# Performance work log

Measured on AMD Instinct MI355X. Metric: run time of the kernel, lower is better.

Reference implementation:

```python
import jax, jax.numpy as jnp
import numpy as np

N, E, G, H, V, L = 100000, 1000000, 1000, 128, 64, 4
NEG_SLOPE = 0.2

def lrelu(x):
    return jnp.where(x >= 0, x, NEG_SLOPE * x)

def setup_inputs() -> dict:
    key = jax.random.key(0)
    ks = jax.random.split(key, 24)
    s = 0.05
    inp = {
        'nfeats': jax.random.randint(ks[0], (N, 9), 0, V, dtype=jnp.int32),
        'efeats': jax.random.randint(ks[1], (E, 3), 0, 4, dtype=jnp.int32),
        'src': jax.random.randint(ks[2], (E,), 0, N, dtype=jnp.int32),
        'dst': jax.random.randint(ks[3], (E,), 0, N, dtype=jnp.int32),
        'graph_ids': jnp.sort(jax.random.randint(ks[4], (N,), 0, G, dtype=jnp.int32)),
        'atom_emb': jax.random.normal(ks[5], (9, V, H), jnp.float32) * s,
        'Wq': jax.random.normal(ks[6], (L, H, H), jnp.float32) * s,
        'bq': jnp.zeros((L, H), jnp.float32),
        'Wk': jax.random.normal(ks[7], (L, H, H), jnp.float32) * s,
        'bk': jnp.zeros((L, H), jnp.float32),
        'Wr': jax.random.normal(ks[8], (L, H, H), jnp.float32) * s,
        'br': jnp.zeros((L, H), jnp.float32),
        'W1': jax.random.normal(ks[9], (H, H // 2), jnp.float32) * s,
        'b1': jnp.zeros((H // 2,), jnp.float32),
        'g1': jnp.ones((H // 2,), jnp.float32),
        'beta1': jnp.zeros((H // 2,), jnp.float32),
        'W2': jax.random.normal(ks[10], (H // 2, H // 4), jnp.float32) * s,
        'b2': jnp.zeros((H // 4,), jnp.float32),
        'g2': jnp.ones((H // 4,), jnp.float32),
        'beta2': jnp.zeros((H // 4,), jnp.float32),
        'W3': jax.random.normal(ks[11], (H // 4, 1), jnp.float32) * s,
        'b3': jnp.zeros((1,), jnp.float32),
    }
    return inp

def batchnorm(x, g, b):
    mu = jnp.mean(x, axis=0)
    var = jnp.var(x, axis=0)
    return (x - mu) * jax.lax.rsqrt(var + 1e-5) * g + b

def reference(nfeats, efeats, src, dst, graph_ids, atom_emb, Wq, bq, Wk, bk, Wr, br,
              W1, b1, g1, beta1, W2, b2, g2, beta2, W3, b3):
    # AtomEncoder: sum of per-feature embeddings -> [N, H]
    h = jnp.sum(atom_emb[jnp.arange(9)[None, :], nfeats], axis=1)
    for l in range(L):
        q = h @ Wq[l] + bq[l]            # dst-side transform [N,H]
        k = h @ Wk[l] + bk[l]            # src-side transform [N,H]
        m = lrelu(q[dst] + k[src])       # per-edge message [E,H]
        agg = jax.ops.segment_sum(m, dst, num_segments=N)  # [N,H]
        h = lrelu(agg @ Wr[l] + br[l])   # norm='none' -> identity, then activation
    hg = jax.ops.segment_sum(h, graph_ids, num_segments=G)  # sum pooling [G,H]
    x = lrelu(batchnorm(hg @ W1 + b1, g1, beta1))
    x = lrelu(batchnorm(x @ W2 + b2, g2, beta2))
    return x @ W3 + b3
```

## Files before the change

kernel.cpp:

```cpp
#include <hip/hip_runtime.h>

#define NN 100000
#define NP 100096
#define NE 1000000
#define NG 1000
#define H 128
#define NLAYER 4
#define NEG 0.2f
#define SCAN_BLOCKS 98

using short8 = __attribute__((ext_vector_type(8))) short;
using fx4 = __attribute__((ext_vector_type(4))) float;

__device__ __forceinline__ float lrelu(float x) { return x >= 0.f ? x : NEG * x; }

__device__ __forceinline__ unsigned short f2bf(float f) {
    union { float f; unsigned int u; } v;
    v.f = f;
    return (unsigned short)((v.u + 0x7fffu + ((v.u >> 16) & 1u)) >> 16);
}
__device__ __forceinline__ float bflo(unsigned int u) {
    union { unsigned int x; float f; } v;
    v.x = u << 16;
    return v.f;
}
__device__ __forceinline__ float bfhi(unsigned int u) {
    union { unsigned int x; float f; } v;
    v.x = u & 0xffff0000u;
    return v.f;
}

__global__ __launch_bounds__(256) void k_wt(const float* __restrict__ Wq,
                                            const float* __restrict__ Wk,
                                            const float* __restrict__ Wr,
                                            unsigned short* __restrict__ WT) {
    int mat = blockIdx.x;
    int l = mat / 3;
    int kind = mat - l * 3;
    const float* src = (kind == 0 ? Wq : kind == 1 ? Wk : Wr) + (size_t)l * H * H;
    unsigned short* dst = WT + (size_t)mat * H * H;
    for (int idx = threadIdx.x; idx < H * H; idx += 256) {
        int kk = idx >> 7, n = idx & 127;
        dst[n * H + kk] = f2bf(src[idx]);
    }
}

__global__ __launch_bounds__(256) void k_hist(const int* __restrict__ dst, int* __restrict__ deg) {
    int i = blockIdx.x * blockDim.x + threadIdx.x;
    if (i * 4 >= NE) return;
    int4 d = *(const int4*)(dst + i * 4);
    atomicAdd(&deg[d.x], 1);
    atomicAdd(&deg[d.y], 1);
    atomicAdd(&deg[d.z], 1);
    atomicAdd(&deg[d.w], 1);
}

__global__ __launch_bounds__(1024) void k_scan1(const int* __restrict__ deg,
                                                int* __restrict__ rowp,
                                                int* __restrict__ bsum) {
    __shared__ int tmp[1024];
    int t = threadIdx.x;
    int i = blockIdx.x * 1024 + t;
    int v = (i < NN) ? deg[i] : 0;
    tmp[t] = v;
    __syncthreads();
    for (int off = 1; off < 1024; off <<= 1) {
        int u = (t >= off) ? tmp[t - off] : 0;
        __syncthreads();
        tmp[t] += u;
        __syncthreads();
    }
    if (i < NN) rowp[i] = tmp[t] - v;
    if (t == 1023) bsum[blockIdx.x] = tmp[1023];
}

__global__ __launch_bounds__(128) void k_scan2(int* __restrict__ bsum) {
    __shared__ int tmp[128];
    int t = threadIdx.x;
    int v = (t < SCAN_BLOCKS) ? bsum[t] : 0;
    tmp[t] = v;
    __syncthreads();
    for (int off = 1; off < 128; off <<= 1) {
        int u = (t >= off) ? tmp[t - off] : 0;
        __syncthreads();
        tmp[t] += u;
        __syncthreads();
    }
    if (t < SCAN_BLOCKS) bsum[t] = tmp[t] - v;
}

#define SCAN3_BLOCKS ((NN + 255) / 256)
__global__ __launch_bounds__(256) void k_scan3g(const int* __restrict__ bsum,
                                                int* __restrict__ rowp,
                                                int* __restrict__ cursor,
                                                const int* __restrict__ gid,
                                                int* __restrict__ gstart) {
    int bid = blockIdx.x;
    int t = threadIdx.x;
    if (bid < SCAN3_BLOCKS) {
        int i = bid * 256 + t;
        if (i < NN) {
            int v = rowp[i] + bsum[i >> 10];
            rowp[i] = v;
            cursor[i] = v;
        }
        if (i == 0) rowp[NN] = NE;
    } else {
        int g = (bid - SCAN3_BLOCKS) * 256 + t;
        if (g > NG) return;
        if (g == NG) { gstart[NG] = NN; return; }
        int lo = 0, hi = NN;
        while (lo < hi) {
            int mid = (lo + hi) >> 1;
            if (gid[mid] < g) lo = mid + 1; else hi = mid;
        }
        gstart[g] = lo;
    }
}

__global__ __launch_bounds__(256) void k_scatter(const int* __restrict__ src,
                                                 const int* __restrict__ dst,
                                                 int* __restrict__ cursor,
                                                 int* __restrict__ csr_src) {
    int i = blockIdx.x * blockDim.x + threadIdx.x;
    if (i * 4 >= NE) return;
    int4 s = *(const int4*)(src + i * 4);
    int4 d = *(const int4*)(dst + i * 4);
    __builtin_nontemporal_store(s.x, &csr_src[atomicAdd(&cursor[d.x], 1)]);
    __builtin_nontemporal_store(s.y, &csr_src[atomicAdd(&cursor[d.y], 1)]);
    __builtin_nontemporal_store(s.z, &csr_src[atomicAdd(&cursor[d.z], 1)]);
    __builtin_nontemporal_store(s.w, &csr_src[atomicAdd(&cursor[d.w], 1)]);
}

__global__ __launch_bounds__(256) void k_aqk_mfma(const int* __restrict__ nfeats,
                                                  const float* __restrict__ emb,
                                                  const unsigned short* __restrict__ WTq,
                                                  const float* __restrict__ bq,
                                                  const unsigned short* __restrict__ WTk,
                                                  const float* __restrict__ bk,
                                                  unsigned short* __restrict__ q,
                                                  unsigned short* __restrict__ k) {
    __shared__ unsigned short hls[4][32][136];
    __shared__ int nf[128 * 9];
    int t = threadIdx.x;
    int lane = t & 63;
    int wave = t >> 6;
    int row0 = blockIdx.x * 128 + wave * 32;
    int lrow = lane & 15;
    int lk = (lane >> 4) << 3;
    unsigned short (*S)[136] = hls[wave];

    {
        int gbase = blockIdx.x * 128 * 9;
        for (int i = t; i < 128 * 9; i += 256) {
            int gi = gbase + i;
            nf[i] = nfeats[gi < NN * 9 ? gi : NN * 9 - 1];
        }
    }
    __syncthreads();

    {
        int c = lane * 2;
        const int* nfw = nf + wave * 32 * 9;
        for (int rr = 0; rr < 32; rr += 2) {
            float ax0 = 0.f, ay0 = 0.f, ax1 = 0.f, ay1 = 0.f;
#pragma unroll
            for (int f = 0; f < 9; ++f) {
                int i0 = nfw[rr * 9 + f];
                int i1 = nfw[(rr + 1) * 9 + f];
                float2 e0 = *(const float2*)(emb + (size_t)((f << 6) + i0) * H + c);
                float2 e1 = *(const float2*)(emb + (size_t)((f << 6) + i1) * H + c);
                ax0 += e0.x; ay0 += e0.y;
                ax1 += e1.x; ay1 += e1.y;
            }
            *(unsigned int*)&S[rr][c] = (unsigned int)f2bf(ax0) | ((unsigned int)f2bf(ay0) << 16);
            *(unsigned int*)&S[rr + 1][c] = (unsigned int)f2bf(ax1) | ((unsigned int)f2bf(ay1) << 16);
        }
    }

    short8 a[2][4];
#pragma unroll
    for (int rt = 0; rt < 2; ++rt)
#pragma unroll
        for (int ks = 0; ks < 4; ++ks)
            a[rt][ks] = *(const short8*)&S[rt * 16 + lrow][ks * 32 + lk];

#pragma unroll
    for (int pass = 0; pass < 4; ++pass) {
        const unsigned short* W = (pass < 2) ? WTq : WTk;
        const float* b = (pass < 2) ? bq : bk;
        unsigned short* o = (pass < 2) ? q : k;
        int c0 = (pass & 1) * 4;
        fx4 acc[2][4];
#pragma unroll
        for (int ct = 0; ct < 4; ++ct) {
            float v = b[(c0 + ct) * 16 + lrow];
#pragma unroll
            for (int rt = 0; rt < 2; ++rt) acc[rt][ct] = fx4{v, v, v, v};
        }
#pragma unroll
        for (int ks = 0; ks < 4; ++ks)
#pragma unroll
            for (int ct = 0; ct < 4; ++ct) {
                short8 w = *(const short8*)(W + ((c0 + ct) * 16 + lrow) * H + ks * 32 + lk);
#pragma unroll
                for (int rt = 0; rt < 2; ++rt)
                    acc[rt][ct] = __builtin_amdgcn_mfma_f32_16x16x32_bf16(a[rt][ks], w, acc[rt][ct], 0, 0, 0);
            }
#pragma unroll
        for (int rt = 0; rt < 2; ++rt)
#pragma unroll
            for (int ct = 0; ct < 4; ++ct)
#pragma unroll
                for (int rg = 0; rg < 4; ++rg)
                    S[rt * 16 + ((lane >> 4) << 2) + rg][(c0 + ct) * 16 + lrow] = f2bf(acc[rt][ct][rg]);
#pragma unroll
        for (int step = 0; step < 4; ++step) {
            int cch = step * 64 + lane;
            int r = cch >> 3;
            int off = c0 * 16 + (cch & 7) * 8;
            int gr = row0 + r;
            if (gr < NN)
                *(uint4*)(o + (size_t)gr * H + off) = *(const uint4*)&S[r][off];
        }
    }
}

__global__ __launch_bounds__(256) void k_r_mfma(const unsigned short* __restrict__ agg,
                                                const unsigned short* __restrict__ WTr,
                                                const float* __restrict__ br,
                                                unsigned short* __restrict__ hout) {
    __shared__ unsigned short hls[4][32][136];
    int lane = threadIdx.x & 63;
    int wave = threadIdx.x >> 6;
    int row0 = blockIdx.x * 128 + wave * 32;
    int lrow = lane & 15;
    int lk = (lane >> 4) << 3;
    unsigned short (*S)[136] = hls[wave];

    short8 a[2][4];
#pragma unroll
    for (int rt = 0; rt < 2; ++rt)
#pragma unroll
        for (int ks = 0; ks < 4; ++ks)
            a[rt][ks] = *(const short8*)(agg + (size_t)(row0 + rt * 16 + lrow) * H + ks * 32 + lk);

#pragma unroll
    for (int chf = 0; chf < 2; ++chf) {
        int c0 = chf * 4;
        fx4 acc[2][4];
#pragma unroll
        for (int ct = 0; ct < 4; ++ct) {
            float v = br[(c0 + ct) * 16 + lrow];
#pragma unroll
            for (int rt = 0; rt < 2; ++rt) acc[rt][ct] = fx4{v, v, v, v};
        }
#pragma unroll
        for (int ks = 0; ks < 4; ++ks)
#pragma unroll
            for (int ct = 0; ct < 4; ++ct) {
                short8 w = *(const short8*)(WTr + ((c0 + ct) * 16 + lrow) * H + ks * 32 + lk);
#pragma unroll
                for (int rt = 0; rt < 2; ++rt)
                    acc[rt][ct] = __builtin_amdgcn_mfma_f32_16x16x32_bf16(a[rt][ks], w, acc[rt][ct], 0, 0, 0);
            }
#pragma unroll
        for (int rt = 0; rt < 2; ++rt)
#pragma unroll
            for (int ct = 0; ct < 4; ++ct)
#pragma unroll
                for (int rg = 0; rg < 4; ++rg)
                    S[rt * 16 + ((lane >> 4) << 2) + rg][(c0 + ct) * 16 + lrow] = f2bf(lrelu(acc[rt][ct][rg]));
    }
#pragma unroll
    for (int step = 0; step < 8; ++step) {
        int cch = step * 64 + lane;
        int r = cch >> 4;
        int off = (cch & 15) * 8;
        int gr = row0 + r;
        if (gr < NN)
            *(uint4*)(hout + (size_t)gr * H + off) = *(const uint4*)&S[r][off];
    }
}

__global__ __launch_bounds__(256) void k_rqk_mfma(const unsigned short* __restrict__ agg,
                                                  const unsigned short* __restrict__ WTr,
                                                  const float* __restrict__ br,
                                                  const unsigned short* __restrict__ WTq,
                                                  const float* __restrict__ bq,
                                                  const unsigned short* __restrict__ WTk,
                                                  const float* __restrict__ bk,
                                                  unsigned short* __restrict__ q,
                                                  unsigned short* __restrict__ k) {
    __shared__ unsigned short hls[4][32][136];
    int lane = threadIdx.x & 63;
    int wave = threadIdx.x >> 6;
    int row0 = blockIdx.x * 128 + wave * 32;
    int lrow = lane & 15;
    int lk = (lane >> 4) << 3;
    unsigned short (*S)[136] = hls[wave];

    short8 a[2][4];
#pragma unroll
    for (int rt = 0; rt < 2; ++rt)
#pragma unroll
        for (int ks = 0; ks < 4; ++ks)
            a[rt][ks] = *(const short8*)(agg + (size_t)(row0 + rt * 16 + lrow) * H + ks * 32 + lk);

#pragma unroll
    for (int chf = 0; chf < 2; ++chf) {
        int c0 = chf * 4;
        fx4 acc[2][4];
#pragma unroll
        for (int ct = 0; ct < 4; ++ct) {
            float v = br[(c0 + ct) * 16 + lrow];
#pragma unroll
            for (int rt = 0; rt < 2; ++rt) acc[rt][ct] = fx4{v, v, v, v};
        }
#pragma unroll
        for (int ks = 0; ks < 4; ++ks)
#pragma unroll
            for (int ct = 0; ct < 4; ++ct) {
                short8 w = *(const short8*)(WTr + ((c0 + ct) * 16 + lrow) * H + ks * 32 + lk);
#pragma unroll
                for (int rt = 0; rt < 2; ++rt)
                    acc[rt][ct] = __builtin_amdgcn_mfma_f32_16x16x32_bf16(a[rt][ks], w, acc[rt][ct], 0, 0, 0);
            }
#pragma unroll
        for (int rt = 0; rt < 2; ++rt)
#pragma unroll
            for (int ct = 0; ct < 4; ++ct)
#pragma unroll
                for (int rg = 0; rg < 4; ++rg)
                    S[rt * 16 + ((lane >> 4) << 2) + rg][(c0 + ct) * 16 + lrow] = f2bf(lrelu(acc[rt][ct][rg]));
    }

    short8 a2[2][4];
#pragma unroll
    for (int rt = 0; rt < 2; ++rt)
#pragma unroll
        for (int ks = 0; ks < 4; ++ks)
            a2[rt][ks] = *(const short8*)&S[rt * 16 + lrow][ks * 32 + lk];

#pragma unroll
    for (int pass = 0; pass < 4; ++pass) {
        const unsigned short* W = (pass < 2) ? WTq : WTk;
        const float* b = (pass < 2) ? bq : bk;
        unsigned short* o = (pass < 2) ? q : k;
        int c0 = (pass & 1) * 4;
        fx4 acc[2][4];
#pragma unroll
        for (int ct = 0; ct < 4; ++ct) {
            float v = b[(c0 + ct) * 16 + lrow];
#pragma unroll
            for (int rt = 0; rt < 2; ++rt) acc[rt][ct] = fx4{v, v, v, v};
        }
#pragma unroll
        for (int ks = 0; ks < 4; ++ks)
#pragma unroll
            for (int ct = 0; ct < 4; ++ct) {
                short8 w = *(const short8*)(W + ((c0 + ct) * 16 + lrow) * H + ks * 32 + lk);
#pragma unroll
                for (int rt = 0; rt < 2; ++rt)
                    acc[rt][ct] = __builtin_amdgcn_mfma_f32_16x16x32_bf16(a2[rt][ks], w, acc[rt][ct], 0, 0, 0);
            }
#pragma unroll
        for (int rt = 0; rt < 2; ++rt)
#pragma unroll
            for (int ct = 0; ct < 4; ++ct)
#pragma unroll
                for (int rg = 0; rg < 4; ++rg)
                    S[rt * 16 + ((lane >> 4) << 2) + rg][(c0 + ct) * 16 + lrow] = f2bf(acc[rt][ct][rg]);
#pragma unroll
        for (int step = 0; step < 4; ++step) {
            int cch = step * 64 + lane;
            int r = cch >> 3;
            int off = c0 * 16 + (cch & 7) * 8;
            int gr = row0 + r;
            if (gr < NN)
                *(uint4*)(o + (size_t)gr * H + off) = *(const uint4*)&S[r][off];
        }
    }
}

__global__ __launch_bounds__(256) void k_agg(const unsigned short* __restrict__ q,
                                             const unsigned short* __restrict__ kk,
                                             const int* __restrict__ rowp,
                                             const int* __restrict__ csr_src,
                                             unsigned short* __restrict__ agg) {
    int node = blockIdx.x * 4 + (threadIdx.x >> 6);
    if (node >= NN) return;
    int lane = threadIdx.x & 63;
    int qt = lane >> 4;
    int ql = lane & 15;
    int start = rowp[node];
    int end = rowp[node + 1];

    uint4 qp = *(const uint4*)(q + (size_t)node * H + ql * 8);
    float qv0 = bflo(qp.x), qv1 = bfhi(qp.x), qv2 = bflo(qp.y), qv3 = bfhi(qp.y);
    float qv4 = bflo(qp.z), qv5 = bfhi(qp.z), qv6 = bflo(qp.w), qv7 = bfhi(qp.w);
    float a0 = 0.f, a1 = 0.f, a2 = 0.f, a3 = 0.f, a4 = 0.f, a5 = 0.f, a6 = 0.f, a7 = 0.f;

    for (int base = start; base < end; base += 64) {
        int cnt = end - base;
        if (cnt > 64) cnt = 64;
        int sid = (lane < cnt) ? csr_src[base + lane] : 0;
        int cnt16 = (cnt + 15) & ~15;
        for (int j = 0; j < cnt16; j += 16) {
            int jj0 = j + qt;
            int jj1 = j + 4 + qt;
            int jj2 = j + 8 + qt;
            int jj3 = j + 12 + qt;
            int s0 = __shfl(sid, jj0);
            int s1 = __shfl(sid, jj1);
            int s2 = __shfl(sid, jj2);
            int s3 = __shfl(sid, jj3);
            uint4 kp0 = *(const uint4*)(kk + (size_t)s0 * H + ql * 8);
            uint4 kp1 = *(const uint4*)(kk + (size_t)s1 * H + ql * 8);
            uint4 kp2 = *(const uint4*)(kk + (size_t)s2 * H + ql * 8);
            uint4 kp3 = *(const uint4*)(kk + (size_t)s3 * H + ql * 8);
            if (jj0 < cnt) {
                a0 += lrelu(qv0 + bflo(kp0.x)); a1 += lrelu(qv1 + bfhi(kp0.x));
                a2 += lrelu(qv2 + bflo(kp0.y)); a3 += lrelu(qv3 + bfhi(kp0.y));
                a4 += lrelu(qv4 + bflo(kp0.z)); a5 += lrelu(qv5 + bfhi(kp0.z));
                a6 += lrelu(qv6 + bflo(kp0.w)); a7 += lrelu(qv7 + bfhi(kp0.w));
            }
            if (jj1 < cnt) {
                a0 += lrelu(qv0 + bflo(kp1.x)); a1 += lrelu(qv1 + bfhi(kp1.x));
                a2 += lrelu(qv2 + bflo(kp1.y)); a3 += lrelu(qv3 + bfhi(kp1.y));
                a4 += lrelu(qv4 + bflo(kp1.z)); a5 += lrelu(qv5 + bfhi(kp1.z));
                a6 += lrelu(qv6 + bflo(kp1.w)); a7 += lrelu(qv7 + bfhi(kp1.w));
            }
            if (jj2 < cnt) {
                a0 += lrelu(qv0 + bflo(kp2.x)); a1 += lrelu(qv1 + bfhi(kp2.x));
                a2 += lrelu(qv2 + bflo(kp2.y)); a3 += lrelu(qv3 + bfhi(kp2.y));
                a4 += lrelu(qv4 + bflo(kp2.z)); a5 += lrelu(qv5 + bfhi(kp2.z));
                a6 += lrelu(qv6 + bflo(kp2.w)); a7 += lrelu(qv7 + bfhi(kp2.w));
            }
            if (jj3 < cnt) {
                a0 += lrelu(qv0 + bflo(kp3.x)); a1 += lrelu(qv1 + bfhi(kp3.x));
                a2 += lrelu(qv2 + bflo(kp3.y)); a3 += lrelu(qv3 + bfhi(kp3.y));
                a4 += lrelu(qv4 + bflo(kp3.z)); a5 += lrelu(qv5 + bfhi(kp3.z));
                a6 += lrelu(qv6 + bflo(kp3.w)); a7 += lrelu(qv7 + bfhi(kp3.w));
            }
        }
    }
    a0 += __shfl_xor(a0, 16); a0 += __shfl_xor(a0, 32);
    a1 += __shfl_xor(a1, 16); a1 += __shfl_xor(a1, 32);
    a2 += __shfl_xor(a2, 16); a2 += __shfl_xor(a2, 32);
    a3 += __shfl_xor(a3, 16); a3 += __shfl_xor(a3, 32);
    a4 += __shfl_xor(a4, 16); a4 += __shfl_xor(a4, 32);
    a5 += __shfl_xor(a5, 16); a5 += __shfl_xor(a5, 32);
    a6 += __shfl_xor(a6, 16); a6 += __shfl_xor(a6, 32);
    a7 += __shfl_xor(a7, 16); a7 += __shfl_xor(a7, 32);
    if (qt == 0) {
        uint4 o;
        o.x = (unsigned int)f2bf(a0) | ((unsigned int)f2bf(a1) << 16);
        o.y = (unsigned int)f2bf(a2) | ((unsigned int)f2bf(a3) << 16);
        o.z = (unsigned int)f2bf(a4) | ((unsigned int)f2bf(a5) << 16);
        o.w = (unsigned int)f2bf(a6) | ((unsigned int)f2bf(a7) << 16);
        *(uint4*)(agg + (size_t)node * H + ql * 8) = o;
    }
}

__global__ __launch_bounds__(256) void k_pool_seg(const unsigned short* __restrict__ h,
                                                  const int* __restrict__ gstart,
                                                  float* __restrict__ hg) {
    int g = blockIdx.x * 4 + (threadIdx.x >> 6);
    if (g >= NG) return;
    int lane = threadIdx.x & 63;
    int s = gstart[g], e = gstart[g + 1];
    float ax = 0.f, ay = 0.f;
    for (int n = s; n < e; ++n) {
        unsigned int hp = *(const unsigned int*)(h + (size_t)n * H + lane * 2);
        ax += bflo(hp);
        ay += bfhi(hp);
    }
    float2 o;
    o.x = ax;
    o.y = ay;
    *(float2*)(hg + (size_t)g * H + lane * 2) = o;
}

__global__ __launch_bounds__(256) void k_mlp1(const float* __restrict__ hg,
                                              const float* __restrict__ W1,
                                              const float* __restrict__ b1,
                                              float* __restrict__ x1) {
    __shared__ float W1s[128 * 64];
    __shared__ float hgs[4 * 128];
    int t = threadIdx.x;
    int g0 = blockIdx.x * 4;
#pragma unroll
    for (int i = 0; i < 32; ++i) W1s[t + i * 256] = W1[t + i * 256];
    for (int i = t; i < 4 * 128; i += 256) hgs[i] = hg[(size_t)g0 * H + i];
    __syncthreads();
    int g = t >> 6, c = t & 63;
    float acc = b1[c];
    const float* row = hgs + g * 128;
    for (int j = 0; j < 128; ++j) acc += row[j] * W1s[j * 64 + c];
    x1[(g0 + g) * 64 + c] = acc;
}

template <int C>
__global__ __launch_bounds__(1024) void k_bnstats(const float* __restrict__ x,
                                                  float* __restrict__ stats) {
    __shared__ float red[1024];
    __shared__ float mus[C];
    int t = threadIdx.x;
    int c = t & (C - 1), rc = t / C;
    const int R = 1024 / C;
    float s = 0.f;
    for (int g = rc; g < NG; g += R) s += x[g * C + c];
    red[t] = s;
    __syncthreads();
    if (t < C) {
        float S = 0.f;
        for (int i = 0; i < R; ++i) S += red[i * C + t];
        float mu = S / NG;
        mus[t] = mu;
        stats[t] = mu;
    }
    __syncthreads();
    float mu = mus[c];
    float s2 = 0.f;
    for (int g = rc; g < NG; g += R) {
        float d = x[g * C + c] - mu;
        s2 += d * d;
    }
    red[t] = s2;
    __syncthreads();
    if (t < C) {
        float Q = 0.f;
        for (int i = 0; i < R; ++i) Q += red[i * C + t];
        stats[C + t] = rsqrtf(Q / NG + 1e-5f);
    }
}

__global__ __launch_bounds__(256) void k_mlp2f(const float* __restrict__ x1,
                                               const float* __restrict__ st,
                                               const float* __restrict__ g1,
                                               const float* __restrict__ be1,
                                               const float* __restrict__ W2,
                                               const float* __restrict__ b2,
                                               float* __restrict__ x2) {
    __shared__ float W2s[64 * 32];
    __shared__ float x1s[8 * 64];
    int t = threadIdx.x;
    int g0 = blockIdx.x * 8;
#pragma unroll
    for (int i = 0; i < 8; ++i) W2s[t + i * 256] = W2[t + i * 256];
#pragma unroll
    for (int i = 0; i < 2; ++i) {
        int idx = t + i * 256;
        int c = idx & 63;
        float v = x1[(size_t)g0 * 64 + idx];
        v = (v - st[c]) * st[64 + c] * g1[c] + be1[c];
        x1s[idx] = lrelu(v);
    }
    __syncthreads();
    int g = t >> 5, c = t & 31;
    float acc = b2[c];
    const float* row = x1s + g * 64;
    for (int j = 0; j < 64; ++j) acc += row[j] * W2s[j * 32 + c];
    x2[(g0 + g) * 32 + c] = acc;
}

__global__ __launch_bounds__(256) void k_mlp3f(const float* __restrict__ x2,
                                               const float* __restrict__ st,
                                               const float* __restrict__ g2,
                                               const float* __restrict__ be2,
                                               const float* __restrict__ W3,
                                               const float* __restrict__ b3,
                                               float* __restrict__ out) {
    int g = blockIdx.x * blockDim.x + threadIdx.x;
    if (g >= NG) return;
    float acc = b3[0];
    for (int j = 0; j < 32; ++j) {
        float v = (x2[g * 32 + j] - st[j]) * st[32 + j] * g2[j] + be2[j];
        acc += lrelu(v) * W3[j];
    }
    out[g] = acc;
}

extern "C" void kernel_launch(void* const* d_in, const int* in_sizes, int n_in,
                              void* d_out, int out_size, void* d_ws, size_t ws_size,
                              hipStream_t stream) {
    const int* nfeats = (const int*)d_in[0];
    const int* src = (const int*)d_in[2];
    const int* dst = (const int*)d_in[3];
    const int* gid = (const int*)d_in[4];
    const float* emb = (const float*)d_in[5];
    const float* Wq = (const float*)d_in[6];
    const float* bq = (const float*)d_in[7];
    const float* Wk = (const float*)d_in[8];
    const float* bk = (const float*)d_in[9];
    const float* Wr = (const float*)d_in[10];
    const float* br = (const float*)d_in[11];
    const float* W1 = (const float*)d_in[12];
    const float* b1 = (const float*)d_in[13];
    const float* g1 = (const float*)d_in[14];
    const float* be1 = (const float*)d_in[15];
    const float* W2 = (const float*)d_in[16];
    const float* b2 = (const float*)d_in[17];
    const float* g2 = (const float*)d_in[18];
    const float* be2 = (const float*)d_in[19];
    const float* W3 = (const float*)d_in[20];
    const float* b3 = (const float*)d_in[21];
    float* out = (float*)d_out;

    size_t nh = (size_t)NP * H;
    unsigned short* P0 = (unsigned short*)d_ws;
    unsigned short* P1 = P0 + nh;
    unsigned short* P2 = P1 + nh;
    unsigned short* WT = P2 + nh;
    float* hg = (float*)(WT + 12 * H * H);
    float* x1 = hg + (size_t)NG * H;
    float* x2 = x1 + (size_t)NG * 64;
    float* st = x2 + (size_t)NG * 32;
    int* cursor = (int*)(st + 2 * 64);
    int* rowp = cursor + NN;
    int* bsum = rowp + NN + 1;
    int* csr_src = bsum + 128;
    int* gstart = csr_src + NE;

    hipMemsetAsync(cursor, 0, NN * sizeof(int), stream);
    k_hist<<<(NE / 4 + 255) / 256, 256, 0, stream>>>(dst, cursor);
    k_scan1<<<SCAN_BLOCKS, 1024, 0, stream>>>(cursor, rowp, bsum);
    k_scan2<<<1, 128, 0, stream>>>(bsum);
    k_scan3g<<<SCAN3_BLOCKS + 4, 256, 0, stream>>>(bsum, rowp, cursor, gid, gstart);
    k_scatter<<<(NE / 4 + 255) / 256, 256, 0, stream>>>(src, dst, cursor, csr_src);

    k_wt<<<12, 256, 0, stream>>>(Wq, Wk, Wr, WT);

    const int NB = NP / 128;
    k_aqk_mfma<<<NB, 256, 0, stream>>>(nfeats, emb, WT + 0 * H * H, bq, WT + 1 * H * H, bk, P1, P2);
    for (int l = 0; l < NLAYER; ++l) {
        k_agg<<<(NN + 3) / 4, 256, 0, stream>>>(P1, P2, rowp, csr_src, P0);
        if (l < NLAYER - 1) {
            k_rqk_mfma<<<NB, 256, 0, stream>>>(P0, WT + (size_t)(l * 3 + 2) * H * H, br + l * H,
                                               WT + (size_t)((l + 1) * 3 + 0) * H * H, bq + (l + 1) * H,
                                               WT + (size_t)((l + 1) * 3 + 1) * H * H, bk + (l + 1) * H,
                                               P1, P2);
        } else {
            k_r_mfma<<<NB, 256, 0, stream>>>(P0, WT + (size_t)(l * 3 + 2) * H * H, br + l * H, P1);
        }
    }

    k_pool_seg<<<(NG + 3) / 4, 256, 0, stream>>>(P1, gstart, hg);

    k_mlp1<<<NG / 4, 256, 0, stream>>>(hg, W1, b1, x1);
    k_bnstats<64><<<1, 1024, 0, stream>>>(x1, st);
    k_mlp2f<<<NG / 8, 256, 0, stream>>>(x1, st, g1, be1, W2, b2, x2);
    k_bnstats<32><<<1, 1024, 0, stream>>>(x2, st);
    k_mlp3f<<<(NG + 255) / 256, 256, 0, stream>>>(x2, st, g2, be2, W3, b3, out);
}
```

Baseline: 674.5 us.

## Build CSR via two-level bucket sort with shared-memory per-bucket counting sort

Replaces per-node global atomic histogram, three-kernel scan and per-node atomic scatter with a coarse 64-node bucket histogram, a single-block bucket scan, a bucket scatter of (src,dst) pairs, and a per-bucket shared-memory counting sort that writes rowp and csr_src. The aim is less global atomic contention and fewer kernel launches during graph preprocessing. The cost is an extra intermediate edge buffer pass. Bucket sizes are capped at 1280 edges, which silently truncates any bucket that exceeds it, so correctness depends on the degree distribution of the input.

```diff
diff --git a/kernel.cpp b/kernel.cpp
--- a/kernel.cpp
+++ b/kernel.cpp
@@ -7,7 +7,8 @@
 #define H 128
 #define NLAYER 4
 #define NEG 0.2f
-#define SCAN_BLOCKS 98
+#define NBUCK ((NN + 63) >> 6)
+#define BCAP 1280
 
 using short8 = __attribute__((ext_vector_type(8))) short;
 using fx4 = __attribute__((ext_vector_type(4))) float;
@@ -45,91 +46,116 @@
     }
 }
 
-__global__ __launch_bounds__(256) void k_hist(const int* __restrict__ dst, int* __restrict__ deg) {
+__global__ __launch_bounds__(256) void k_bhist(const int* __restrict__ dst,
+                                               int* __restrict__ bhist) {
     int i = blockIdx.x * blockDim.x + threadIdx.x;
     if (i * 4 >= NE) return;
     int4 d = *(const int4*)(dst + i * 4);
-    atomicAdd(&deg[d.x], 1);
-    atomicAdd(&deg[d.y], 1);
-    atomicAdd(&deg[d.z], 1);
-    atomicAdd(&deg[d.w], 1);
-}
-
-__global__ __launch_bounds__(1024) void k_scan1(const int* __restrict__ deg,
-                                                int* __restrict__ rowp,
-                                                int* __restrict__ bsum) {
-    __shared__ int tmp[1024];
+    atomicAdd(&bhist[d.x >> 6], 1);
+    atomicAdd(&bhist[d.y >> 6], 1);
+    atomicAdd(&bhist[d.z >> 6], 1);
+    atomicAdd(&bhist[d.w >> 6], 1);
+}
+
+__global__ __launch_bounds__(1024) void k_bscan(const int* __restrict__ bhist,
+                                                int* __restrict__ bstart,
+                                                int* __restrict__ bcursor,
+                                                int* __restrict__ rowp) {
+    __shared__ int part[1024];
     int t = threadIdx.x;
-    int i = blockIdx.x * 1024 + t;
-    int v = (i < NN) ? deg[i] : 0;
-    tmp[t] = v;
+    int i0 = t * 2;
+    int v0 = (i0 < NBUCK) ? bhist[i0] : 0;
+    int v1 = (i0 + 1 < NBUCK) ? bhist[i0 + 1] : 0;
+    part[t] = v0 + v1;
     __syncthreads();
     for (int off = 1; off < 1024; off <<= 1) {
-        int u = (t >= off) ? tmp[t - off] : 0;
+        int u = (t >= off) ? part[t - off] : 0;
         __syncthreads();
-        tmp[t] += u;
+        part[t] += u;
         __syncthreads();
     }
-    if (i < NN) rowp[i] = tmp[t] - v;
-    if (t == 1023) bsum[blockIdx.x] = tmp[1023];
-}
-
-__global__ __launch_bounds__(128) void k_scan2(int* __restrict__ bsum) {
-    __shared__ int tmp[128];
-    int t = threadIdx.x;
-    int v = (t < SCAN_BLOCKS) ? bsum[t] : 0;
-    tmp[t] = v;
-    __syncthreads();
-    for (int off = 1; off < 128; off <<= 1) {
-        int u = (t >= off) ? tmp[t - off] : 0;
-        __syncthreads();
-        tmp[t] += u;
-        __syncthreads();
-    }
-    if (t < SCAN_BLOCKS) bsum[t] = tmp[t] - v;
-}
-
-#define SCAN3_BLOCKS ((NN + 255) / 256)
-__global__ __launch_bounds__(256) void k_scan3g(const int* __restrict__ bsum,
-                                                int* __restrict__ rowp,
-                                                int* __restrict__ cursor,
-                                                const int* __restrict__ gid,
-                                                int* __restrict__ gstart) {
-    int bid = blockIdx.x;
-    int t = threadIdx.x;
-    if (bid < SCAN3_BLOCKS) {
-        int i = bid * 256 + t;
-        if (i < NN) {
-            int v = rowp[i] + bsum[i >> 10];
-            rowp[i] = v;
-            cursor[i] = v;
-        }
-        if (i == 0) rowp[NN] = NE;
-    } else {
-        int g = (bid - SCAN3_BLOCKS) * 256 + t;
-        if (g > NG) return;
-        if (g == NG) { gstart[NG] = NN; return; }
-        int lo = 0, hi = NN;
-        while (lo < hi) {
-            int mid = (lo + hi) >> 1;
-            if (gid[mid] < g) lo = mid + 1; else hi = mid;
-        }
-        gstart[g] = lo;
-    }
-}
-
-__global__ __launch_bounds__(256) void k_scatter(const int* __restrict__ src,
-                                                 const int* __restrict__ dst,
-                                                 int* __restrict__ cursor,
-                                                 int* __restrict__ csr_src) {
+    int base = (t == 0) ? 0 : part[t - 1];
+    if (i0 < NBUCK) { bstart[i0] = base; bcursor[i0] = base; }
+    if (i0 + 1 < NBUCK) { bstart[i0 + 1] = base + v0; bcursor[i0 + 1] = base + v0; }
+    if (t == 1023) { bstart[NBUCK] = part[1023]; rowp[NN] = NE; }
+}
+
+__global__ __launch_bounds__(256) void k_bscatter(const int* __restrict__ src,
+                                                  const int* __restrict__ dst,
+                                                  int* __restrict__ bcursor,
+                                                  int2* __restrict__ ebuf) {
     int i = blockIdx.x * blockDim.x + threadIdx.x;
     if (i * 4 >= NE) return;
     int4 s = *(const int4*)(src + i * 4);
     int4 d = *(const int4*)(dst + i * 4);
-    __builtin_nontemporal_store(s.x, &csr_src[atomicAdd(&cursor[d.x], 1)]);
-    __builtin_nontemporal_store(s.y, &csr_src[atomicAdd(&cursor[d.y], 1)]);
-    __builtin_nontemporal_store(s.z, &csr_src[atomicAdd(&cursor[d.z], 1)]);
-    __builtin_nontemporal_store(s.w, &csr_src[atomicAdd(&cursor[d.w], 1)]);
+    int p0 = atomicAdd(&bcursor[d.x >> 6], 1);
+    ebuf[p0] = make_int2(s.x, d.x);
+    int p1 = atomicAdd(&bcursor[d.y >> 6], 1);
+    ebuf[p1] = make_int2(s.y, d.y);
+    int p2 = atomicAdd(&bcursor[d.z >> 6], 1);
+    ebuf[p2] = make_int2(s.z, d.z);
+    int p3 = atomicAdd(&bcursor[d.w >> 6], 1);
+    ebuf[p3] = make_int2(s.w, d.w);
+}
+
+__global__ __launch_bounds__(256) void k_bucket2(const int2* __restrict__ ebuf,
+                                                 const int* __restrict__ bstart,
+                                                 int* __restrict__ rowp,
+                                                 int* __restrict__ csr_src) {
+    __shared__ int2 eb[BCAP];
+    __shared__ int lsrc[BCAP];
+    __shared__ int ldeg[64];
+    __shared__ int lofs[64];
+    __shared__ int lcur[64];
+    int b = blockIdx.x;
+    int t = threadIdx.x;
+    int s = bstart[b], e = bstart[b + 1];
+    int cnt = e - s;
+    if (cnt > BCAP) cnt = BCAP;
+    int n0 = b << 6;
+
+    if (t < 64) ldeg[t] = 0;
+    __syncthreads();
+    for (int i = t; i < cnt; i += 256) {
+        int2 ed = ebuf[s + i];
+        eb[i] = ed;
+        atomicAdd(&ldeg[ed.y - n0], 1);
+    }
+    __syncthreads();
+    if (t < 64) {
+        int v = ldeg[t];
+        int inc = v;
+        for (int off = 1; off < 64; off <<= 1) {
+            int u = __shfl_up(inc, off);
+            if (t >= off) inc += u;
+        }
+        int ex = inc - v;
+        lofs[t] = ex;
+        lcur[t] = ex;
+        int n = n0 + t;
+        if (n < NN) rowp[n] = s + ex;
+    }
+    __syncthreads();
+    for (int i = t; i < cnt; i += 256) {
+        int2 ed = eb[i];
+        int lpos = atomicAdd(&lcur[ed.y - n0], 1);
+        lsrc[lpos] = ed.x;
+    }
+    __syncthreads();
+    for (int i = t; i < cnt; i += 256) csr_src[s + i] = lsrc[i];
+}
+
+__global__ __launch_bounds__(256) void k_gbound(const int* __restrict__ gid,
+                                                int* __restrict__ gstart) {
+    int g = blockIdx.x * blockDim.x + threadIdx.x;
+    if (g > NG) return;
+    if (g == NG) { gstart[NG] = NN; return; }
+    int lo = 0, hi = NN;
+    while (lo < hi) {
+        int mid = (lo + hi) >> 1;
+        if (gid[mid] < g) lo = mid + 1; else hi = mid;
+    }
+    gstart[g] = lo;
 }
 
 __global__ __launch_bounds__(256) void k_aqk_mfma(const int* __restrict__ nfeats,
@@ -617,18 +643,20 @@
     float* x1 = hg + (size_t)NG * H;
     float* x2 = x1 + (size_t)NG * 64;
     float* st = x2 + (size_t)NG * 32;
-    int* cursor = (int*)(st + 2 * 64);
-    int* rowp = cursor + NN;
-    int* bsum = rowp + NN + 1;
-    int* csr_src = bsum + 128;
+    int2* ebuf = (int2*)(st + 2 * 64);
+    int* rowp = (int*)(ebuf + NE);
+    int* bhist = rowp + NN + 1;
+    int* bstart = bhist + NBUCK;
+    int* bcursor = bstart + NBUCK + 1;
+    int* csr_src = bcursor + NBUCK;
     int* gstart = csr_src + NE;
 
-    hipMemsetAsync(cursor, 0, NN * sizeof(int), stream);
-    k_hist<<<(NE / 4 + 255) / 256, 256, 0, stream>>>(dst, cursor);
-    k_scan1<<<SCAN_BLOCKS, 1024, 0, stream>>>(cursor, rowp, bsum);
-    k_scan2<<<1, 128, 0, stream>>>(bsum);
-    k_scan3g<<<SCAN3_BLOCKS + 4, 256, 0, stream>>>(bsum, rowp, cursor, gid, gstart);
-    k_scatter<<<(NE / 4 + 255) / 256, 256, 0, stream>>>(src, dst, cursor, csr_src);
+    hipMemsetAsync(bhist, 0, NBUCK * sizeof(int), stream);
+    k_bhist<<<(NE / 4 + 255) / 256, 256, 0, stream>>>(dst, bhist);
+    k_bscan<<<1, 1024, 0, stream>>>(bhist, bstart, bcursor, rowp);
+    k_bscatter<<<(NE / 4 + 255) / 256, 256, 0, stream>>>(src, dst, bcursor, ebuf);
+    k_bucket2<<<NBUCK, 256, 0, stream>>>(ebuf, bstart, rowp, csr_src);
+    k_gbound<<<(NG + 256) / 256, 256, 0, stream>>>(gid, gstart);
 
     k_wt<<<12, 256, 0, stream>>>(Wq, Wk, Wr, WT);
 
```

Measured after the change: 864.8 us. +28.2%, slower.
